# Performance work log

Measured on AMD Instinct MI355X. Metric: run time of the kernel, lower is better.

## Reference

```python
import jax, jax.numpy as jnp
import numpy as np
import math

B, L, HID = 2, 2048, 1024
NH, DH = 16, 64
MASK_VAL = -1000000000.0  # half_precision_flag == False


def setup_inputs() -> dict:
    key = jax.random.key(0)
    ks = jax.random.split(key, 12)
    s = 0.02
    return {
        "queries": jax.random.normal(ks[0], (B, L, HID), jnp.float32),
        "keys": jax.random.normal(ks[1], (B, L, HID), jnp.float32),
        "values": jax.random.normal(ks[2], (B, L, HID), jnp.float32),
        "mask": jax.random.randint(ks[3], (B, L, L), 0, 2, jnp.int32),
        "Wq": jax.random.normal(ks[4], (HID, NH * DH), jnp.float32) * s,
        "bq": jnp.zeros((NH * DH,), jnp.float32),
        "Wk": jax.random.normal(ks[5], (HID, NH * DH), jnp.float32) * s,
        "bk": jnp.zeros((NH * DH,), jnp.float32),
        "Wv": jax.random.normal(ks[6], (HID, NH * DH), jnp.float32) * s,
        "bv": jnp.zeros((NH * DH,), jnp.float32),
        "Wo": jax.random.normal(ks[7], (NH * DH, HID), jnp.float32) * s,
        "bo": jnp.zeros((HID,), jnp.float32),
    }


def reference(queries, keys, values, mask, Wq, bq, Wk, bk, Wv, bv, Wo, bo):
    # Linear projections: (B, L, NH*DH)
    q = queries @ Wq + bq
    k = keys @ Wk + bk
    v = values @ Wv + bv
    # FAITHFUL to original: raw .view(B, NH, -1, DH) without transpose
    q = q.reshape(B, NH, L, DH)
    k = k.reshape(B, NH, L, DH)
    v = v.reshape(B, NH, L, DH)
    # scaled dot-product scores: (B, NH, L, L)
    scores = jnp.einsum("bhqd,bhkd->bhqk", q, k) / math.sqrt(DH)
    scores = jnp.where(mask[:, None, :, :] == 0, MASK_VAL, scores)
    probs = jax.nn.softmax(scores, axis=-1)  # dropout p=0 -> identity
    ctx = jnp.einsum("bhqk,bhkd->bhqd", probs, v)  # (B, NH, L, DH)
    # transpose(1,2) then flatten heads, as in original
    ctx = ctx.transpose(0, 2, 1, 3).reshape(B, L, NH * DH)
    return ctx @ Wo + bo
```

## Files before the change

### kernel.cpp

```cpp
#include <hip/hip_runtime.h>
#include <stdint.h>

typedef __bf16 bf16;
typedef __bf16 bf16x8 __attribute__((ext_vector_type(8)));
typedef __bf16 bf16x4 __attribute__((ext_vector_type(4)));
typedef __bf16 bf16x2 __attribute__((ext_vector_type(2)));
typedef float  f32x4  __attribute__((ext_vector_type(4)));
typedef float  f32x16 __attribute__((ext_vector_type(16)));
typedef short  s16x4  __attribute__((ext_vector_type(4)));
typedef short  s16x8  __attribute__((ext_vector_type(8)));
typedef unsigned int u32x2 __attribute__((ext_vector_type(2)));
typedef unsigned int u32x4 __attribute__((ext_vector_type(4)));
typedef unsigned long long ull;

#define GLOAD16(gptr, lptr)                                                     \
  __builtin_amdgcn_global_load_lds(                                             \
      (const __attribute__((address_space(1))) void*)(gptr),                    \
      (__attribute__((address_space(3))) void*)(lptr), 16, 0, 0)

#define MFMA16(a, b, c) __builtin_amdgcn_mfma_f32_16x16x32_bf16((a), (b), (c), 0, 0, 0)
#define MFMA32(a, b, c) __builtin_amdgcn_mfma_f32_32x32x16_bf16((a), (b), (c), 0, 0, 0)

static constexpr int B_ = 2, L_ = 2048, NH_ = 16, DH_ = 64;
static constexpr float QSCALE = 0.18033688011112042f;

__global__ __launch_bounds__(256) void k_prep(const float* __restrict__ q,
                                              const float* __restrict__ k,
                                              const float* __restrict__ v,
                                              const int* __restrict__ mask,
                                              const float* __restrict__ wq,
                                              const float* __restrict__ wk,
                                              const float* __restrict__ wv,
                                              const float* __restrict__ wo,
                                              bf16* __restrict__ X,
                                              bf16* __restrict__ Wt,
                                              ull* __restrict__ mb) {
  __shared__ float t[32][33];
  const int bid = blockIdx.x, tid = threadIdx.x;
  if (bid < 2048) {
#pragma unroll
    for (int it = 0; it < 16; ++it) {
      int tt = (bid * 16 + it) * 256 + tid;
      ull bal = __ballot(mask[tt] != 0);
      if ((tid & 63) == 0) mb[tt >> 6] = bal;
    }
  } else if (bid < 4096) {
    const int u0 = (bid - 2048) * 6;
#pragma unroll
    for (int it = 0; it < 6; ++it) {
      int u = u0 + it;
      int z = u >> 12, x = u & 4095;
      const float* in = z == 0 ? q : (z == 1 ? k : v);
      bf16* out = X + (size_t)z * 4194304;
      int i = x * 256 + tid;
      const float4 f = ((const float4*)in)[i];
      bf16x4 o = {(bf16)f.x, (bf16)f.y, (bf16)f.z, (bf16)f.w};
      ((bf16x4*)out)[i] = o;
    }
  } else {
    const int t0 = (bid - 4096) * 4;
    for (int it = 0; it < 4; ++it) {
      int u = t0 + it;
      int z = u >> 10, rem = u & 1023;
      const float* in = z == 0 ? wq : (z == 1 ? wk : (z == 2 ? wv : wo));
      bf16* out = Wt + (size_t)z * 1048576;
      int bx = (rem & 31) * 32, by = (rem >> 5) * 32;
      int x = tid & 31, y = tid >> 5;
#pragma unroll
      for (int r = 0; r < 4; ++r)
        t[y + r * 8][x] = in[(size_t)(by + y + r * 8) * 1024 + bx + x];
      __syncthreads();
#pragma unroll
      for (int r = 0; r < 4; ++r)
        out[(size_t)(bx + y + r * 8) * 1024 + by + x] = (bf16)t[x][y + r * 8];
      __syncthreads();
    }
  }
}

__global__ __launch_bounds__(256) void k_gemm3(const bf16* __restrict__ Xb,
                                               const bf16* __restrict__ Wb,
                                               const float* __restrict__ b0,
                                               const float* __restrict__ b1,
                                               const float* __restrict__ b2,
                                               bf16* __restrict__ Ob) {
  const int lin = blockIdx.x;
  const int cx = lin & 7, j = (lin >> 3) & 7, gg = lin >> 6;
  const int g = gg * 8 + cx;
  const int y = g & 31, z = g >> 5;
  const int m0 = y * 128, n0 = j * 128;
  const bf16* A  = Xb + (size_t)z * 4194304;
  const bf16* Bt = Wb + (size_t)z * 1048576;
  const float* bias = z == 0 ? b0 : (z == 1 ? b1 : b2);
  bf16* C = Ob + (size_t)z * 4194304;
  __shared__ __align__(16) bf16 As[128 * 32];
  __shared__ __align__(16) bf16 Bs[128 * 32];
  const int tid = threadIdx.x, lane = tid & 63, w = tid >> 6, quad = lane >> 4, l15 = lane & 15;
  const int wm = (w & 1) * 64, wn = (w >> 1) * 64;
  f32x4 acc[4][4] = {};
  for (int kt = 0; kt < 32; ++kt) {
    const int kk = kt * 32;
#pragma unroll
    for (int i = 0; i < 2; ++i) {
      int s = tid + i * 256;
      int r = s >> 2, c = (s & 3) ^ ((r >> 1) & 3);
      GLOAD16(A + (size_t)(m0 + r) * 1024 + kk + c * 8, As + s * 8);
      GLOAD16(Bt + (size_t)(n0 + r) * 1024 + kk + c * 8, Bs + s * 8);
    }
    __syncthreads();
    bf16x8 af[4], bb[4];
#pragma unroll
    for (int i = 0; i < 4; ++i) {
      int ra = wm + i * 16 + l15, rb = wn + i * 16 + l15;
      af[i] = *(const bf16x8*)(As + (ra * 4 + (quad ^ ((ra >> 1) & 3))) * 8);
      bb[i] = *(const bf16x8*)(Bs + (rb * 4 + (quad ^ ((rb >> 1) & 3))) * 8);
    }
#pragma unroll
    for (int mi = 0; mi < 4; ++mi)
#pragma unroll
      for (int ni = 0; ni < 4; ++ni)
        acc[mi][ni] = MFMA16(af[mi], bb[ni], acc[mi][ni]);
    __syncthreads();
  }
  const float scale = (z == 0) ? QSCALE : 1.0f;
#pragma unroll
  for (int mi = 0; mi < 4; ++mi)
#pragma unroll
    for (int ni = 0; ni < 4; ++ni) {
      int row = m0 + wm + mi * 16 + quad * 4;
      int col = n0 + wn + ni * 16 + l15;
      float bz = bias[col];
      if (z == 2) {
        int b_ = row >> 11, l = row & 2047;
        int hh = l >> 7;
        int i0 = (l & 127) * 16 + (col >> 6);
        int d  = col & 63;
        bf16* dst = C + (size_t)(b_ * 16 + hh) * 131072;
#pragma unroll
        for (int r = 0; r < 4; ++r) {
          int iK = i0 + 16 * r;
          dst[((size_t)(iK >> 3) * 64 + d) * 8 + (iK & 7)] = (bf16)(acc[mi][ni][r] + bz);
        }
      } else {
#pragma unroll
        for (int r = 0; r < 4; ++r)
          C[(size_t)(row + r) * 1024 + col] = (bf16)((acc[mi][ni][r] + bz) * scale);
      }
    }
}

__global__ __launch_bounds__(256) void k_gemmo(const bf16* __restrict__ A,
                                               const bf16* __restrict__ Bt,
                                               const float* __restrict__ bias,
                                               float* __restrict__ C) {
  const int lin = blockIdx.x;
  const int cx = lin & 7, j = (lin >> 3) & 7, gg = lin >> 6;
  const int y = gg * 8 + cx;
  const int m0 = y * 64, n0 = j * 128;
  __shared__ __align__(16) bf16 As[64 * 32];
  __shared__ __align__(16) bf16 Bs[128 * 32];
  const int tid = threadIdx.x, lane = tid & 63, w = tid >> 6, quad = lane >> 4, l15 = lane & 15;
  const int wn = w * 32;
  f32x4 acc[4][2] = {};
  for (int kt = 0; kt < 32; ++kt) {
    const int kk = kt * 32;
    {
      int r = tid >> 2, c = (tid & 3) ^ ((r >> 1) & 3);
      GLOAD16(A + (size_t)(m0 + r) * 1024 + kk + c * 8, As + tid * 8);
    }
#pragma unroll
    for (int i = 0; i < 2; ++i) {
      int s = tid + i * 256;
      int r = s >> 2, c = (s & 3) ^ ((r >> 1) & 3);
      GLOAD16(Bt + (size_t)(n0 + r) * 1024 + kk + c * 8, Bs + s * 8);
    }
    __syncthreads();
    bf16x8 af[4], bb[2];
#pragma unroll
    for (int i = 0; i < 4; ++i) {
      int ra = i * 16 + l15;
      af[i] = *(const bf16x8*)(As + (ra * 4 + (quad ^ ((ra >> 1) & 3))) * 8);
    }
#pragma unroll
    for (int i = 0; i < 2; ++i) {
      int rb = wn + i * 16 + l15;
      bb[i] = *(const bf16x8*)(Bs + (rb * 4 + (quad ^ ((rb >> 1) & 3))) * 8);
    }
#pragma unroll
    for (int mi = 0; mi < 4; ++mi)
#pragma unroll
      for (int ni = 0; ni < 2; ++ni)
        acc[mi][ni] = MFMA16(af[mi], bb[ni], acc[mi][ni]);
    __syncthreads();
  }
#pragma unroll
  for (int mi = 0; mi < 4; ++mi)
#pragma unroll
    for (int ni = 0; ni < 2; ++ni) {
      int row = m0 + mi * 16 + quad * 4;
      int col = n0 + wn + ni * 16 + l15;
      float bz = bias[col];
#pragma unroll
      for (int r = 0; r < 4; ++r)
        C[(size_t)(row + r) * 1024 + col] = acc[mi][ni][r] + bz;
    }
}

static __device__ __forceinline__ unsigned pack2(float a, float b) {
  bf16x2 t = {(bf16)a, (bf16)b};
  return __builtin_bit_cast(unsigned, t);
}

static __device__ __forceinline__ void flash_step(
    const bf16* __restrict__ Kc, const bf16* __restrict__ Vc, unsigned mw32,
    const bf16x8 (&qf)[4], bf16x8 ones8,
    int hi, int keyq, int swz, int vo0, int vo1, int vo2, int vo3,
    f32x16& accO0, f32x16& accO1, f32x16& accL) {
  bf16x8 v0 = *(const bf16x8*)(Vc + vo0);
  bf16x8 v1 = *(const bf16x8*)(Vc + vo1);
  bf16x8 v2 = *(const bf16x8*)(Vc + vo2);
  bf16x8 v3 = *(const bf16x8*)(Vc + vo3);

  f32x16 st = {};
  __builtin_amdgcn_s_setprio(1);
#pragma unroll
  for (int ks = 0; ks < 4; ++ks) {
    bf16x8 kf = *(const bf16x8*)(Kc + (keyq * 8 + ((ks * 2 + hi) ^ swz)) * 8);
    st = MFMA32(kf, qf[ks], st);
  }
  __builtin_amdgcn_s_setprio(0);

#pragma unroll
  for (int r = 0; r < 16; ++r) {
    const int bit = (r >> 2) * 8 + (r & 3);
    st[r] = (mw32 >> bit) & 1u ? __builtin_amdgcn_exp2f(st[r]) : 0.f;
  }

  bf16x8 af0, af1;
  {
    unsigned c0 = pack2(st[0], st[1]);
    unsigned c1 = pack2(st[2], st[3]);
    unsigned c2 = pack2(st[4], st[5]);
    unsigned c3 = pack2(st[6], st[7]);
    u32x2 s0 = __builtin_amdgcn_permlane32_swap(c0, c2, false, false);
    u32x2 s1 = __builtin_amdgcn_permlane32_swap(c1, c3, false, false);
    u32x4 a4 = {s0.x, s1.x, s0.y, s1.y};
    af0 = __builtin_bit_cast(bf16x8, a4);
    c0 = pack2(st[8], st[9]);
    c1 = pack2(st[10], st[11]);
    c2 = pack2(st[12], st[13]);
    c3 = pack2(st[14], st[15]);
    s0 = __builtin_amdgcn_permlane32_swap(c0, c2, false, false);
    s1 = __builtin_amdgcn_permlane32_swap(c1, c3, false, false);
    u32x4 b4 = {s0.x, s1.x, s0.y, s1.y};
    af1 = __builtin_bit_cast(bf16x8, b4);
  }

  __builtin_amdgcn_s_setprio(1);
  accL  = MFMA32(af0, ones8, accL);
  accL  = MFMA32(af1, ones8, accL);
  accO0 = MFMA32(af0, v0, accO0);
  accO1 = MFMA32(af0, v1, accO1);
  accO0 = MFMA32(af1, v2, accO0);
  accO1 = MFMA32(af1, v3, accO1);
  __builtin_amdgcn_s_setprio(0);
}

__global__ __launch_bounds__(512) void k_flash(const bf16* __restrict__ Qp,
                                               const bf16* __restrict__ Kp,
                                               const bf16* __restrict__ Vtp,
                                               const ull* __restrict__ mb,
                                               bf16* __restrict__ ctx) {
  const int b = blockIdx.z, h = blockIdx.y, q0 = blockIdx.x * 128;
  const size_t HEAD = 131072;
  const bf16* Q  = Qp  + ((size_t)b * NH_ + h) * HEAD;
  const bf16* K  = Kp  + ((size_t)b * NH_ + h) * HEAD;
  const bf16* Vt = Vtp + ((size_t)b * NH_ + h) * HEAD;
  const ull* mrow = mb + (size_t)b * L_ * 32;

  __shared__ __align__(16) unsigned char RAW[36864];
  bf16* Ksb = (bf16*)RAW;
  bf16* Vsb = (bf16*)(RAW + 16384);
  ull*  Msb = (ull*)(RAW + 32768);
  const unsigned* Ms32 = (const unsigned*)(RAW + 32768);

  const int tid = threadIdx.x, lane = tid & 63, w = tid >> 6;
  const int hi = lane >> 5, l31 = lane & 31;
  const int kh = w & 1, qq = w >> 1;
  const int keyq = kh * 32 + l31;
  const int swz = (keyq ^ (keyq >> 3)) & 7;
  const int vo0 = ((kh * 4 + hi) * 64 + l31) * 8;
  const int vo1 = vo0 + 256;
  const int vo2 = vo0 + 1024;
  const int vo3 = vo2 + 256;

  bf16x8 qf[4];
  {
    const bf16* qrow = Q + (size_t)(q0 + qq * 32 + l31) * 64 + hi * 8;
    qf[0] = *(const bf16x8*)(qrow);
    qf[1] = *(const bf16x8*)(qrow + 16);
    qf[2] = *(const bf16x8*)(qrow + 32);
    qf[3] = *(const bf16x8*)(qrow + 48);
  }

#define STAGE(T, SL)                                                            \
  {                                                                             \
    int s_ = tid, key_ = s_ >> 3, c_ = (s_ & 7) ^ ((key_ ^ (key_ >> 3)) & 7);   \
    GLOAD16(K + ((size_t)(T) * 64 + key_) * 64 + c_ * 8, Ksb + (SL) * 4096 + s_ * 8); \
    GLOAD16(Vt + (size_t)(T) * 4096 + s_ * 8, Vsb + (SL) * 4096 + s_ * 8);      \
  }

  STAGE(0, 0);
  if (w < 2) {
    int r = w * 64 + lane;
    GLOAD16(mrow + (size_t)(q0 + r) * 32, (bf16*)Msb + r * 8);
  }
  __syncthreads();

  f32x16 accO0 = {}, accO1 = {}, accL = {};
  const s16x8 one8s = {0x3F80, 0x3F80, 0x3F80, 0x3F80, 0x3F80, 0x3F80, 0x3F80, 0x3F80};
  const bf16x8 ones8 = __builtin_bit_cast(bf16x8, one8s);

  for (int kt = 0; kt < 32; ++kt) {
    const int cur = kt & 1;
    if (kt + 1 < 32) {
      STAGE(kt + 1, cur ^ 1);
      if ((kt & 1) && w < 2) {
        int r = w * 64 + lane;
        GLOAD16(mrow + (size_t)(q0 + r) * 32 + (kt + 1),
                (bf16*)Msb + (((kt + 1) >> 1) & 1) * 1024 + r * 8);
      }
    }
    const unsigned mw32 =
        Ms32[((((kt >> 1) & 1) * 256 + (qq * 32 + l31) * 2 + cur) << 1) + kh] >> (4 * hi);
    flash_step(Ksb + cur * 4096, Vsb + cur * 4096, mw32, qf, ones8, hi, keyq, swz,
               vo0, vo1, vo2, vo3, accO0, accO1, accL);
    __syncthreads();
  }
#undef STAGE

  float* red  = (float*)RAW;
  float* redL = (float*)(RAW + 32768);
  if (kh == 1) {
#pragma unroll
    for (int r = 0; r < 16; ++r) {
      const int qrel = (r & 3) + 8 * (r >> 2) + 4 * hi;
      red[qq * 2048 + qrel * 64 + l31]      = accO0[r];
      red[qq * 2048 + qrel * 64 + 32 + l31] = accO1[r];
      if (l31 == 0) redL[qq * 32 + qrel] = accL[r];
    }
  }
  __syncthreads();
  if (kh == 0) {
#pragma unroll
    for (int r = 0; r < 16; ++r) {
      const int qrel = (r & 3) + 8 * (r >> 2) + 4 * hi;
      const float ls = accL[r] + redL[qq * 32 + qrel];
      const float rl = 1.0f / ls;
      const float o0 = accO0[r] + red[qq * 2048 + qrel * 64 + l31];
      const float o1 = accO1[r] + red[qq * 2048 + qrel * 64 + 32 + l31];
      const int rowg = q0 + qq * 32 + qrel;
      ctx[((size_t)b * L_ + rowg) * 1024 + h * 64 + l31]      = (bf16)(o0 * rl);
      ctx[((size_t)b * L_ + rowg) * 1024 + h * 64 + 32 + l31] = (bf16)(o1 * rl);
    }
  }
}

extern "C" void kernel_launch(void* const* d_in, const int* in_sizes, int n_in,
                              void* d_out, int out_size, void* d_ws, size_t ws_size,
                              hipStream_t stream) {
  (void)in_sizes; (void)n_in; (void)out_size; (void)ws_size;
  const float* q    = (const float*)d_in[0];
  const float* k    = (const float*)d_in[1];
  const float* v    = (const float*)d_in[2];
  const int*   mask = (const int*)d_in[3];
  const float* Wq = (const float*)d_in[4];
  const float* bq = (const float*)d_in[5];
  const float* Wk = (const float*)d_in[6];
  const float* bk = (const float*)d_in[7];
  const float* Wv = (const float*)d_in[8];
  const float* bv = (const float*)d_in[9];
  const float* Wo = (const float*)d_in[10];
  const float* bo = (const float*)d_in[11];
  float* out = (float*)d_out;

  char* ws = (char*)d_ws;
  const size_t SX = (size_t)4096 * 1024 * 2;
  const size_t SW = (size_t)1024 * 1024 * 2;
  bf16* X   = (bf16*)(ws);
  bf16* Wt  = (bf16*)(ws + 3 * SX);
  bf16* QKV = (bf16*)(ws + 3 * SX + 4 * SW);
  bf16* Qp  = QKV;
  bf16* Kp  = QKV + 4194304;
  bf16* Vtp = QKV + 2 * 4194304;
  bf16* Ctx = (bf16*)(ws + 6 * SX + 4 * SW);
  ull* mbits = (ull*)(ws + 7 * SX + 4 * SW);

  dim3 blk(256);
  k_prep<<<5120, blk, 0, stream>>>(q, k, v, mask, Wq, Wk, Wv, Wo, X, Wt, mbits);

  k_gemm3<<<768, blk, 0, stream>>>(X, Wt, bq, bk, bv, QKV);

  k_flash<<<dim3(16, NH_, B_), dim3(512), 0, stream>>>(Qp, Kp, Vtp, mbits, Ctx);

  k_gemmo<<<512, blk, 0, stream>>>(Ctx, Wt + 3 * 1048576, bo, out);
}
```

Measured before the change: 256.5 us.

## Process two key tiles per barrier and load mask bits directly to registers

The flash kernel now stages two K/V tiles per iteration into a four-slot shared buffer (64KB), halving the number of block-wide barriers per key sweep. Mask words are read straight from global memory into registers one group ahead, replacing the shared-memory mask staging. This cuts synchronization overhead, but the larger shared allocation may lower occupancy, and the per-lane scattered mask loads may be less efficient.

```diff
diff --git a/kernel.cpp b/kernel.cpp
--- a/kernel.cpp
+++ b/kernel.cpp
@@ -269,20 +269,17 @@
 __global__ __launch_bounds__(512) void k_flash(const bf16* __restrict__ Qp,
                                                const bf16* __restrict__ Kp,
                                                const bf16* __restrict__ Vtp,
-                                               const ull* __restrict__ mb,
+                                               const unsigned* __restrict__ mb32,
                                                bf16* __restrict__ ctx) {
   const int b = blockIdx.z, h = blockIdx.y, q0 = blockIdx.x * 128;
   const size_t HEAD = 131072;
   const bf16* Q  = Qp  + ((size_t)b * NH_ + h) * HEAD;
   const bf16* K  = Kp  + ((size_t)b * NH_ + h) * HEAD;
   const bf16* Vt = Vtp + ((size_t)b * NH_ + h) * HEAD;
-  const ull* mrow = mb + (size_t)b * L_ * 32;
-
-  __shared__ __align__(16) unsigned char RAW[36864];
+
+  __shared__ __align__(16) unsigned char RAW[65536];
   bf16* Ksb = (bf16*)RAW;
-  bf16* Vsb = (bf16*)(RAW + 16384);
-  ull*  Msb = (ull*)(RAW + 32768);
-  const unsigned* Ms32 = (const unsigned*)(RAW + 32768);
+  bf16* Vsb = (bf16*)(RAW + 32768);
 
   const int tid = threadIdx.x, lane = tid & 63, w = tid >> 6;
   const int hi = lane >> 5, l31 = lane & 31;
@@ -294,6 +291,8 @@
   const int vo2 = vo0 + 1024;
   const int vo3 = vo2 + 256;
 
+  const unsigned* mrow = mb32 + ((size_t)b * L_ + q0 + qq * 32 + l31) * 64 + kh;
+
   bf16x8 qf[4];
   {
     const bf16* qrow = Q + (size_t)(q0 + qq * 32 + l31) * 64 + hi * 8;
@@ -310,30 +309,28 @@
     GLOAD16(Vt + (size_t)(T) * 4096 + s_ * 8, Vsb + (SL) * 4096 + s_ * 8);      \
   }
 
+  unsigned mA = mrow[0], mB = mrow[2];
   STAGE(0, 0);
-  if (w < 2) {
-    int r = w * 64 + lane;
-    GLOAD16(mrow + (size_t)(q0 + r) * 32, (bf16*)Msb + r * 8);
-  }
+  STAGE(1, 1);
   __syncthreads();
 
   f32x16 accO0 = {}, accO1 = {}, accL = {};
   const s16x8 one8s = {0x3F80, 0x3F80, 0x3F80, 0x3F80, 0x3F80, 0x3F80, 0x3F80, 0x3F80};
   const bf16x8 ones8 = __builtin_bit_cast(bf16x8, one8s);
 
-  for (int kt = 0; kt < 32; ++kt) {
-    const int cur = kt & 1;
-    if (kt + 1 < 32) {
-      STAGE(kt + 1, cur ^ 1);
-      if ((kt & 1) && w < 2) {
-        int r = w * 64 + lane;
-        GLOAD16(mrow + (size_t)(q0 + r) * 32 + (kt + 1),
-                (bf16*)Msb + (((kt + 1) >> 1) & 1) * 1024 + r * 8);
-      }
-    }
-    const unsigned mw32 =
-        Ms32[((((kt >> 1) & 1) * 256 + (qq * 32 + l31) * 2 + cur) << 1) + kh] >> (4 * hi);
-    flash_step(Ksb + cur * 4096, Vsb + cur * 4096, mw32, qf, ones8, hi, keyq, swz,
+  for (int g = 0; g < 16; ++g) {
+    const int cs = (g & 1) * 2;
+    const unsigned cm0 = mA >> (4 * hi);
+    const unsigned cm1 = mB >> (4 * hi);
+    if (g < 15) {
+      mA = mrow[(2 * g + 2) * 2];
+      mB = mrow[(2 * g + 3) * 2];
+      STAGE(2 * g + 2, cs ^ 2);
+      STAGE(2 * g + 3, (cs ^ 2) + 1);
+    }
+    flash_step(Ksb + cs * 4096, Vsb + cs * 4096, cm0, qf, ones8, hi, keyq, swz,
+               vo0, vo1, vo2, vo3, accO0, accO1, accL);
+    flash_step(Ksb + (cs + 1) * 4096, Vsb + (cs + 1) * 4096, cm1, qf, ones8, hi, keyq, swz,
                vo0, vo1, vo2, vo3, accO0, accO1, accL);
     __syncthreads();
   }
@@ -401,7 +398,7 @@
 
   k_gemm3<<<768, blk, 0, stream>>>(X, Wt, bq, bk, bv, QKV);
 
-  k_flash<<<dim3(16, NH_, B_), dim3(512), 0, stream>>>(Qp, Kp, Vtp, mbits, Ctx);
+  k_flash<<<dim3(16, NH_, B_), dim3(512), 0, stream>>>(Qp, Kp, Vtp, (const unsigned*)mbits, Ctx);
 
   k_gemmo<<<512, blk, 0, stream>>>(Ctx, Wt + 3 * 1048576, bo, out);
 }
```

Measured after the change: 270.3 us. 1.05x slower.
